# Optimization experiments

Hardware: AMD Instinct MI355X
Metric: run time of the kernel (lower is better)

Reference implementation:

```python
import jax, jax.numpy as jnp
import numpy as np

FIX_SCALE = np.array([[0.,0.,0.],[1.,0.,0.],[0.,1.,0.],[0.,0.,1.],[-1.,0.,0.],[0.,-1.,0.]], dtype=np.float32)
NUM_HEADS = 8
ATTN_DIMS = 512
HEAD_DIMS = ATTN_DIMS // NUM_HEADS
NUM_LEARN = 6
SIG_CLAMP = 9.21  # safe_sigmoid clamp


def quat_to_rotmat(q):
    # q: [G,4] (w,x,y,z), normalized -> [G,3,3]
    q = q / jnp.linalg.norm(q, axis=-1, keepdims=True)
    w, x, y, z = q[..., 0], q[..., 1], q[..., 2], q[..., 3]
    r0 = jnp.stack([1 - 2*(y*y + z*z), 2*(x*y - w*z), 2*(x*z + w*y)], -1)
    r1 = jnp.stack([2*(x*y + w*z), 1 - 2*(x*x + z*z), 2*(y*z - w*x)], -1)
    r2 = jnp.stack([2*(x*z - w*y), 2*(y*z + w*x), 1 - 2*(x*x + y*y)], -1)
    return jnp.stack([r0, r1, r2], -2)


def bilinear_sample(fm, gx, gy):
    # fm: [C,H,W]; gx,gy: [...] in [-1,1]; align_corners=False, zero padding
    C, H, W = fm.shape
    x = (gx + 1.0) * (W * 0.5) - 0.5
    y = (gy + 1.0) * (H * 0.5) - 0.5
    x0 = jnp.floor(x); y0 = jnp.floor(y)
    wx1 = x - x0; wx0 = 1.0 - wx1
    wy1 = y - y0; wy0 = 1.0 - wy1

    def gather(xf, yf):
        xi = xf.astype(jnp.int32); yi = yf.astype(jnp.int32)
        valid = (xi >= 0) & (xi < W) & (yi >= 0) & (yi < H)
        xi = jnp.clip(xi, 0, W - 1); yi = jnp.clip(yi, 0, H - 1)
        return fm[:, yi, xi] * valid[None].astype(fm.dtype)  # [C, ...]

    out = (gather(x0, y0) * (wx0 * wy0)[None]
           + gather(x0 + 1, y0) * (wx1 * wy0)[None]
           + gather(x0, y0 + 1) * (wx0 * wy1)[None]
           + gather(x0 + 1, y0 + 1) * (wx1 * wy1)[None])
    return jnp.moveaxis(out, 0, -1)  # [..., C]


def setup_inputs() -> dict:
    key = jax.random.key(0)
    ks = jax.random.split(key, 16)
    G, BS, GFD = 8192, 1, 32
    means = jax.random.uniform(ks[0], (G, 3), minval=-1.0, maxval=1.0)
    means = means.at[:, 2].add(3.0)  # push in front of camera
    scales = jax.random.uniform(ks[1], (G, 3), minval=0.01, maxval=0.1)
    rotations = jax.random.normal(ks[2], (G, 4))
    features = jax.random.normal(ks[3], (BS, G, 3, GFD))
    transforms = jnp.tile(jnp.eye(4)[None], (G, 1, 1)) + 0.01 * jax.random.normal(ks[4], (G, 4, 4))
    f = 64.0
    proj = jnp.array([[f, 0., 32., 0.], [0., f, 32., 0.], [0., 0., 1., 0.], [0., 0., 0., 1.]], dtype=jnp.float32)
    projection = jnp.tile(proj[None], (BS, 1, 1))
    image_features = jax.random.normal(ks[5], (BS, 256, 64, 64))
    s = lambda d: 1.0 / np.sqrt(d)
    Wq = jax.random.normal(ks[6], (GFD, ATTN_DIMS)) * s(GFD)
    Wk = jax.random.normal(ks[7], (ATTN_DIMS, 256)) * s(256)
    Wv = jax.random.normal(ks[8], (ATTN_DIMS, 256)) * s(256)
    W_off = jax.random.normal(ks[9], (HEAD_DIMS + 3, NUM_LEARN * 3)) * s(HEAD_DIMS + 3)
    b_off = jnp.zeros((NUM_LEARN * 3,))
    Wout = jax.random.normal(ks[10], (ATTN_DIMS, GFD)) * s(ATTN_DIMS)
    b_out = jnp.zeros((GFD,))
    return {"means": means, "scales": scales, "rotations": rotations, "features": features,
            "transforms": transforms, "projection": projection, "image_features": image_features,
            "Wq": Wq, "Wk": Wk, "Wv": Wv, "W_off": W_off, "b_off": b_off, "Wout": Wout, "b_out": b_out}


def reference(means, scales, rotations, features, transforms, projection, image_features,
              Wq, Wk, Wv, W_off, b_off, Wout, b_out):
    G = means.shape[0]
    bs = features.shape[0]
    H, HD = NUM_HEADS, HEAD_DIMS
    h_img, w_img = image_features.shape[-2:]

    # queries: [bs,G,3,attn] -> [bs,H,G,3,hd]
    q_full = jnp.einsum('bgtf,fa->bgta', features, Wq)
    q = q_full.reshape(bs, G, 3, H, HD).transpose(0, 3, 1, 2, 4)

    # transform means to world space with per-gaussian 4x4
    homo = jnp.concatenate([means, jnp.ones((G, 1), means.dtype)], -1)  # [G,4]
    means_w = jnp.einsum('gij,gj->gi', transforms, homo)[:, :3]  # [G,3]

    # OffsetNet: per-head learnable offsets from (world mean, token-mean query)
    q_mean = q.mean(axis=3)  # [bs,H,G,hd]
    m_b = jnp.broadcast_to(means_w[None, None], (bs, H, G, 3))
    off_in = jnp.concatenate([m_b, q_mean], -1)  # [bs,H,G,hd+3]
    learnable = jax.nn.sigmoid(jnp.clip(off_in @ W_off + b_off, -SIG_CLAMP, SIG_CLAMP))
    learnable = learnable.reshape(bs, H, G, NUM_LEARN, 3) - 0.5
    fix = jnp.broadcast_to(jnp.asarray(FIX_SCALE)[None, None, None], (bs, H, G, FIX_SCALE.shape[0], 3))
    scale_all = jnp.concatenate([fix, learnable], axis=-2)  # [bs,H,G,K,3]
    K = scale_all.shape[-2]

    offset_pts = scale_all * scales[None, None, :, None, :]
    RT = jnp.swapaxes(quat_to_rotmat(rotations), -1, -2)  # [G,3,3]
    offset_pts = jnp.einsum('gij,bhgkj->bhgki', RT, offset_pts) + means_w[None, None, :, None, :]

    # project to 2D, normalize to [0,1), then to grid coords [-1,1]
    pts4 = jnp.concatenate([offset_pts, jnp.ones_like(offset_pts[..., :1])], -1)
    p = jnp.einsum('bij,bhgkj->bhgki', projection, pts4)
    p2 = p[..., :2] / jnp.clip(p[..., 2:3], 1e-5)
    wh = jnp.array([w_img, h_img], dtype=p2.dtype)
    pnorm = jnp.clip(p2 / wh, 0.0, 0.9999)
    grid = 2.0 * pnorm - 1.0  # [bs,H,G,K,2]

    # key/value maps via 1x1 conv, split into per-head channel groups
    kmap = jnp.einsum('ac,bchw->bahw', Wk, image_features).reshape(bs, H, HD, h_img, w_img)
    vmap_ = jnp.einsum('ac,bchw->bahw', Wv, image_features).reshape(bs, H, HD, h_img, w_img)

    sample_bh = jax.vmap(jax.vmap(bilinear_sample, in_axes=(0, 0, 0)), in_axes=(0, 0, 0))
    k_s = sample_bh(kmap, grid[..., 0], grid[..., 1])   # [bs,H,G,K,hd]
    v_s = sample_bh(vmap_, grid[..., 0], grid[..., 1])  # [bs,H,G,K,hd]

    scale = HD ** -0.5
    scores = jnp.einsum('bhgid,bhgkd->bhgik', q, k_s) * scale
    attn = jax.nn.softmax(scores, axis=-1)
    out = jnp.einsum('bhgik,bhgkd->bhgid', attn, v_s)  # [bs,H,G,3,hd]
    out = out.transpose(0, 2, 3, 1, 4).reshape(bs, G, 3, H * HD)  # b g i (h d)
    out = out @ Wout + b_out
    return out + features
```

## Files before the change

### kernel.cpp

```cpp
#include <hip/hip_runtime.h>
#include <hip/hip_bf16.h>
#include <hip/hip_fp16.h>

typedef _Float16 half2v __attribute__((ext_vector_type(2)));
typedef _Float16 half8v __attribute__((ext_vector_type(8)));
typedef __attribute__((ext_vector_type(4))) float float4v;

__device__ __forceinline__ half2v u2h(unsigned u) { return __builtin_bit_cast(half2v, u); }
__device__ __forceinline__ unsigned h2u(half2v h) { return __builtin_bit_cast(unsigned, h); }
__device__ __forceinline__ unsigned short f2hu(float f) {
    _Float16 h = (_Float16)f; return __builtin_bit_cast(unsigned short, h);
}
__device__ __forceinline__ unsigned packh(float lo, float hi) {
    half2v h; h[0] = (_Float16)lo; h[1] = (_Float16)hi; return h2u(h);
}
__device__ __forceinline__ void ld8h(const unsigned short* p, float* f) {
    uint4 u = *(const uint4*)p;
    half2v h0 = u2h(u.x), h1 = u2h(u.y), h2 = u2h(u.z), h3 = u2h(u.w);
    f[0] = (float)h0[0]; f[1] = (float)h0[1]; f[2] = (float)h1[0]; f[3] = (float)h1[1];
    f[4] = (float)h2[0]; f[5] = (float)h2[1]; f[6] = (float)h3[0]; f[7] = (float)h3[1];
}

__global__ __launch_bounds__(256) void offmlp_kernel(
    const float* __restrict__ means, const float* __restrict__ transforms,
    const float* __restrict__ features, const float* __restrict__ Wq,
    const float* __restrict__ W_off, const float* __restrict__ b_off,
    float* __restrict__ lrn_all)
{
    __shared__ __attribute__((aligned(16))) unsigned short Wq16[32 * 512];
    __shared__ float Woffs[1224];
    __shared__ float Wc[36][144];
    __shared__ float A[32][38];
    const int tid = threadIdx.x;
    const int g0 = blockIdx.x * 32;

#pragma unroll
    for (int i = 0; i < 16; i++) {
        int idx4 = i * 256 + tid;
        float4 v = ((const float4*)Wq)[idx4];
        unsigned* dst = (unsigned*)&Wq16[idx4 * 4];
        dst[0] = packh(v.x, v.y);
        dst[1] = packh(v.z, v.w);
    }
    for (int i = tid; i < 1206; i += 256) Woffs[i] = W_off[i];
    if (tid < 18) Woffs[1206 + tid] = b_off[tid];
    {
        const int gi = tid >> 3, sl = tid & 7;
        const int g = g0 + gi;
        const float* fb = features + (size_t)g * 96 + sl * 4;
        float4 t0 = *(const float4*)(fb);
        float4 t1 = *(const float4*)(fb + 32);
        float4 t2 = *(const float4*)(fb + 64);
        A[gi][3 + sl * 4 + 0] = (t0.x + t1.x + t2.x) * (1.f / 3.f);
        A[gi][3 + sl * 4 + 1] = (t0.y + t1.y + t2.y) * (1.f / 3.f);
        A[gi][3 + sl * 4 + 2] = (t0.z + t1.z + t2.z) * (1.f / 3.f);
        A[gi][3 + sl * 4 + 3] = (t0.w + t1.w + t2.w) * (1.f / 3.f);
        if (sl < 3) {
            const float* T = transforms + (size_t)g * 16 + sl * 4;
            float m0 = means[(size_t)g * 3];
            float m1 = means[(size_t)g * 3 + 1];
            float m2 = means[(size_t)g * 3 + 2];
            A[gi][sl] = T[0] * m0 + T[1] * m1 + T[2] * m2 + T[3];
        } else if (sl == 3) {
            A[gi][35] = 1.f;
        }
    }
    __syncthreads();

    for (int k = 0; k < 21; k++) {
        int oi = k * 256 + tid;
        if (oi < 5184) {
            int j = oi / 144, c = oi - j * 144;
            int h = c / 18, l = c - h * 18;
            float v;
            if (j < 3) {
                v = Woffs[j * 18 + l];
            } else if (j == 35) {
                v = Woffs[1206 + l];
            } else {
                int f = j - 3;
                const unsigned* wq2 = (const unsigned*)&Wq16[f * 512 + h * 64];
                float s = 0.f;
#pragma unroll
                for (int d2 = 0; d2 < 32; d2++) {
                    half2v w2 = u2h(wq2[d2]);
                    s += (float)w2[0] * Woffs[(3 + 2 * d2) * 18 + l]
                       + (float)w2[1] * Woffs[(4 + 2 * d2) * 18 + l];
                }
                v = s;
            }
            Wc[j][c] = v;
        }
    }
    __syncthreads();

#pragma unroll
    for (int k = 0; k < 18; k++) {
        int oi = k * 256 + tid;
        int gi = oi / 144, c = oi - gi * 144;
        float s = 0.f;
#pragma unroll
        for (int j = 0; j < 36; j++) s += A[gi][j] * Wc[j][c];
        s = fminf(fmaxf(s, -9.21f), 9.21f);
        lrn_all[(size_t)(g0 + gi) * 144 + c] = 1.f / (1.f + expf(-s)) - 0.5f;
    }
}

__global__ __launch_bounds__(256) void conv_fused_kernel(
    const float* __restrict__ img, const float* __restrict__ Wk,
    const float* __restrict__ Wv, unsigned short* __restrict__ buf)
{
    __shared__ __attribute__((aligned(16))) unsigned short Bt[64][264];
    __shared__ __attribute__((aligned(16))) unsigned short Wt[64][264];
    const int tid = threadIdx.x;
    const int p0 = blockIdx.x * 64;

#pragma unroll
    for (int i = 0; i < 4; i++) {
        int chunk = i * 256 + tid;
        int kp  = chunk >> 3;
        int pxg = (chunk & 7) * 8;
        const float* r0 = img + (size_t)(2 * kp) * 4096 + p0 + pxg;
        const float* r1 = img + (size_t)(2 * kp + 1) * 4096 + p0 + pxg;
        float4 a0 = *(const float4*)r0, a1 = *(const float4*)(r0 + 4);
        float4 b0 = *(const float4*)r1, b1 = *(const float4*)(r1 + 4);
        unsigned lo[8], hi[8];
        lo[0] = f2hu(a0.x); lo[1] = f2hu(a0.y); lo[2] = f2hu(a0.z); lo[3] = f2hu(a0.w);
        lo[4] = f2hu(a1.x); lo[5] = f2hu(a1.y); lo[6] = f2hu(a1.z); lo[7] = f2hu(a1.w);
        hi[0] = f2hu(b0.x); hi[1] = f2hu(b0.y); hi[2] = f2hu(b0.z); hi[3] = f2hu(b0.w);
        hi[4] = f2hu(b1.x); hi[5] = f2hu(b1.y); hi[6] = f2hu(b1.z); hi[7] = f2hu(b1.w);
#pragma unroll
        for (int j = 0; j < 8; j++)
            *(unsigned*)&Bt[pxg + j][2 * kp] = lo[j] | (hi[j] << 16);
    }

    const int w = tid >> 6, l = tid & 63;
    const int m = l & 15, quad = l >> 4;
    const int mrow = w * 16 + m;

#pragma unroll
    for (int j = 0; j < 2; j++) {
        const int o0 = blockIdx.y * 128 + j * 64;
        const float* Wsel = (o0 < 512) ? Wk : Wv;
        const int obase = (o0 < 512) ? o0 : (o0 - 512);
        if (j) __syncthreads();
        {
            const int row = tid >> 2, q = tid & 3;
            const float* wp = Wsel + (size_t)(obase + row) * 256 + q * 64;
#pragma unroll
            for (int jj = 0; jj < 8; jj++) {
                float4 w0 = *(const float4*)(wp + jj * 8);
                float4 w1 = *(const float4*)(wp + jj * 8 + 4);
                uint4 pk;
                pk.x = packh(w0.x, w0.y); pk.y = packh(w0.z, w0.w);
                pk.z = packh(w1.x, w1.y); pk.w = packh(w1.z, w1.w);
                *(uint4*)&Wt[row][q * 64 + jj * 8] = pk;
            }
        }
        __syncthreads();

        float4v acc[4] = {{0,0,0,0},{0,0,0,0},{0,0,0,0},{0,0,0,0}};
#pragma unroll
        for (int kk = 0; kk < 8; kk++) {
            const int kofs = kk * 32 + quad * 8;
            half8v af = *(const half8v*)&Bt[mrow][kofs];
#pragma unroll
            for (int nt = 0; nt < 4; nt++) {
                half8v b8 = *(const half8v*)&Wt[nt * 16 + m][kofs];
                acc[nt] = __builtin_amdgcn_mfma_f32_16x16x32_f16(af, b8, acc[nt], 0, 0, 0);
            }
        }
#pragma unroll
        for (int nt = 0; nt < 4; nt++) {
#pragma unroll
            for (int r = 0; r < 4; r++) {
                size_t px = p0 + w * 16 + quad * 4 + r;
                buf[px * 1024 + o0 + nt * 16 + m] = f2hu(acc[nt][r]);
            }
        }
    }
}

__global__ __launch_bounds__(256) void qgemm_kernel(
    const float* __restrict__ features, const float* __restrict__ Wq,
    unsigned short* __restrict__ qfull)
{
    __shared__ __attribute__((aligned(16))) unsigned short WqT[256][40];
    const int tid = threadIdx.x;
    const int R0 = blockIdx.x * 64;
    const int n0 = blockIdx.y * 256;
#pragma unroll
    for (int k = 0; k < 32; k++)
        WqT[tid][k] = f2hu(Wq[(size_t)k * 512 + n0 + tid]);
    __syncthreads();

    const int w = tid >> 6, l = tid & 63, m = l & 15, quad = l >> 4;
    const int row = R0 + w * 16 + m;
    const float* fp = features + (size_t)row * 32 + quad * 8;
    float4 f0 = *(const float4*)fp, f1 = *(const float4*)(fp + 4);
    half8v af;
    af[0] = (_Float16)f0.x; af[1] = (_Float16)f0.y;
    af[2] = (_Float16)f0.z; af[3] = (_Float16)f0.w;
    af[4] = (_Float16)f1.x; af[5] = (_Float16)f1.y;
    af[6] = (_Float16)f1.z; af[7] = (_Float16)f1.w;
    float4v acc[16];
#pragma unroll
    for (int t = 0; t < 16; t++) acc[t] = (float4v){0.f, 0.f, 0.f, 0.f};
#pragma unroll
    for (int t = 0; t < 16; t++) {
        half8v b8 = *(const half8v*)&WqT[t * 16 + m][quad * 8];
        acc[t] = __builtin_amdgcn_mfma_f32_16x16x32_f16(af, b8, acc[t], 0, 0, 0);
    }
    const int rb = R0 + w * 16 + quad * 4;
#pragma unroll
    for (int t = 0; t < 16; t++)
#pragma unroll
        for (int r = 0; r < 4; r++)
            qfull[(size_t)(rb + r) * 512 + n0 + t * 16 + m] = f2hu(acc[t][r]);
}

__global__ __launch_bounds__(256, 4) void attn_core_kernel(
    const float* __restrict__ means, const float* __restrict__ scales,
    const float* __restrict__ rot,   const float* __restrict__ transforms,
    const float* __restrict__ projection, const float* __restrict__ lrn_all,
    const unsigned short* __restrict__ buf, unsigned short* __restrict__ qfull)
{
    __shared__ __attribute__((aligned(16))) unsigned qf2[768];
    __shared__ __attribute__((aligned(16))) unsigned vsh2[3072];
    __shared__ __attribute__((aligned(16))) uint4 pixwt[96];
    __shared__ __attribute__((aligned(16))) unsigned att2[288];
    __shared__ __attribute__((aligned(16))) float lrnsh[144];
    __shared__ float mw[3], sc3[3], Rt[9], pr[12];

    const int g = blockIdx.x, tid = threadIdx.x;

    if (tid < 36) {
        ((float4*)lrnsh)[tid] = ((const float4*)(lrn_all + (size_t)g * 144))[tid];
    }
    if (tid >= 64 && tid < 67) {
        sc3[tid - 64] = scales[(size_t)g * 3 + (tid - 64)];
    } else if (tid >= 68 && tid < 80) {
        pr[tid - 68] = projection[tid - 68];
    } else if (tid == 80) {
        float w = rot[(size_t)g * 4],     x = rot[(size_t)g * 4 + 1];
        float y = rot[(size_t)g * 4 + 2], z = rot[(size_t)g * 4 + 3];
        float n = rsqrtf(w * w + x * x + y * y + z * z);
        w *= n; x *= n; y *= n; z *= n;
        float R00 = 1 - 2 * (y * y + z * z), R01 = 2 * (x * y - w * z), R02 = 2 * (x * z + w * y);
        float R10 = 2 * (x * y + w * z), R11 = 1 - 2 * (x * x + z * z), R12 = 2 * (y * z - w * x);
        float R20 = 2 * (x * z - w * y), R21 = 2 * (y * z + w * x), R22 = 1 - 2 * (x * x + y * y);
        Rt[0] = R00; Rt[1] = R10; Rt[2] = R20;
        Rt[3] = R01; Rt[4] = R11; Rt[5] = R21;
        Rt[6] = R02; Rt[7] = R12; Rt[8] = R22;
    } else if (tid >= 84 && tid < 87) {
        int i = tid - 84;
        float m0 = means[(size_t)g * 3];
        float m1 = means[(size_t)g * 3 + 1];
        float m2 = means[(size_t)g * 3 + 2];
        const float* T = transforms + (size_t)g * 16 + i * 4;
        mw[i] = T[0] * m0 + T[1] * m1 + T[2] * m2 + T[3];
    }
    {
        const unsigned* qsrc = (const unsigned*)(qfull + (size_t)g * 1536);
#pragma unroll
        for (int i = 0; i < 3; i++) qf2[tid + i * 256] = qsrc[tid + i * 256];
    }
    __syncthreads();

    if (tid < 96) {
        int h = tid / 12, k = tid % 12;
        float s0, s1, s2;
        if (k < 6) {
            const float FSx[6] = {0.f, 1.f, 0.f, 0.f, -1.f, 0.f};
            const float FSy[6] = {0.f, 0.f, 1.f, 0.f, 0.f, -1.f};
            const float FSz[6] = {0.f, 0.f, 0.f, 1.f, 0.f, 0.f};
            s0 = FSx[k]; s1 = FSy[k]; s2 = FSz[k];
        } else {
            int b = h * 18 + (k - 6) * 3;
            s0 = lrnsh[b]; s1 = lrnsh[b + 1]; s2 = lrnsh[b + 2];
        }
        float o0 = s0 * sc3[0], o1 = s1 * sc3[1], o2 = s2 * sc3[2];
        float wx = Rt[0] * o0 + Rt[1] * o1 + Rt[2] * o2 + mw[0];
        float wy = Rt[3] * o0 + Rt[4] * o1 + Rt[5] * o2 + mw[1];
        float wz = Rt[6] * o0 + Rt[7] * o1 + Rt[8] * o2 + mw[2];
        float px = pr[0] * wx + pr[1] * wy + pr[2]  * wz + pr[3];
        float py = pr[4] * wx + pr[5] * wy + pr[6]  * wz + pr[7];
        float pz = pr[8] * wx + pr[9] * wy + pr[10] * wz + pr[11];
        pz = fmaxf(pz, 1e-5f);
        float gx = fminf(fmaxf(px / pz * (1.f / 64.f), 0.f), 0.9999f);
        float gy = fminf(fmaxf(py / pz * (1.f / 64.f), 0.f), 0.9999f);
        float x = gx * 64.f - 0.5f, y = gy * 64.f - 0.5f;
        float fx = floorf(x), fy = floorf(y);
        int x0 = (int)fx, y0 = (int)fy;
        float wx1 = x - fx, wy1 = y - fy;
        float wx0 = 1.f - wx1, wy0 = 1.f - wy1;
        int xs[2] = {x0, x0 + 1}, ys[2] = {y0, y0 + 1};
        float wxs[2] = {wx0, wx1}, wys[2] = {wy0, wy1};
        unsigned pix[4]; float wf[4];
#pragma unroll
        for (int c = 0; c < 4; c++) {
            int xi = xs[c & 1], yi = ys[c >> 1];
            bool v = ((unsigned)xi < 64u) & ((unsigned)yi < 64u);
            int xc = min(max(xi, 0), 63), yc = min(max(yi, 0), 63);
            pix[c] = (unsigned)(yc * 64 + xc);
            wf[c] = v ? wxs[c & 1] * wys[c >> 1] : 0.f;
        }
        uint4 pw;
        pw.x = pix[0] | (pix[1] << 16);
        pw.y = pix[2] | (pix[3] << 16);
        pw.z = packh(wf[0], wf[1]);
        pw.w = packh(wf[2], wf[3]);
        pixwt[tid] = pw;
// ... 72 lines not shown
    if (tid < 24) {
        float*    row  = (float*)att2 + tid * 12;
        unsigned* rowp = att2 + tid * 12;
        float m = row[0];
#pragma unroll
        for (int k = 1; k < 12; k++) m = fmaxf(m, row[k]);
        float e_[12]; float ssum = 0.f;
#pragma unroll
        for (int k = 0; k < 12; k++) { e_[k] = expf(row[k] - m); ssum += e_[k]; }
        float inv = 1.f / ssum;
#pragma unroll
        for (int k = 0; k < 12; k++) { float a = e_[k] * inv; rowp[k] = packh(a, a); }
    }
    __syncthreads();

    {
        unsigned* oa32 = (unsigned*)(qfull + (size_t)g * 1536);
#pragma unroll
        for (int i = 0; i < 3; i++) {
            int e = tid + i * 256;
            int t = e >> 8, a2p = e & 255;
            int h = a2p >> 5, ddp = a2p & 31;
            const unsigned* ar2 = att2 + (h * 3 + t) * 12;
            const unsigned* vp  = vsh2 + h * 12 * 32 + ddp;
            half2v acc = {0, 0};
#pragma unroll
            for (int k = 0; k < 12; k++)
                acc += u2h(ar2[k]) * u2h(vp[k * 32]);
            oa32[e] = h2u(acc);
        }
    }
}

__global__ __launch_bounds__(256, 6) void attn_core_basic(
    const float* __restrict__ means, const float* __restrict__ scales,
    const float* __restrict__ rot,   const float* __restrict__ transforms,
    const float* __restrict__ projection, const float* __restrict__ W_off,
    const float* __restrict__ b_off, const unsigned short* __restrict__ buf,
    unsigned short* __restrict__ qfull)
{
    __shared__ __attribute__((aligned(16))) unsigned qf2[768];
    __shared__ __attribute__((aligned(16))) unsigned vsh2[3072];
    __shared__ __attribute__((aligned(16))) float qm_u[512];
    __shared__ __attribute__((aligned(16))) unsigned att2[288];
    __shared__ float mw[3], sc3[3], Rt[9], pr[12];

    float* lrn  = (float*)att2;
    float* wofl = (float*)vsh2;
    float* bofl = wofl + 1206;

    const int g = blockIdx.x, tid = threadIdx.x;

    for (int i = tid; i < 1206; i += 256) wofl[i] = W_off[i];
    if (tid < 18) bofl[tid] = b_off[tid];
    if (tid >= 32 && tid < 35) {
        sc3[tid - 32] = scales[(size_t)g * 3 + (tid - 32)];
    } else if (tid >= 36 && tid < 48) {
        pr[tid - 36] = projection[tid - 36];
    } else if (tid == 48) {
        float w = rot[(size_t)g * 4],     x = rot[(size_t)g * 4 + 1];
        float y = rot[(size_t)g * 4 + 2], z = rot[(size_t)g * 4 + 3];
        float n = rsqrtf(w * w + x * x + y * y + z * z);
        w *= n; x *= n; y *= n; z *= n;
        float R00 = 1 - 2 * (y * y + z * z), R01 = 2 * (x * y - w * z), R02 = 2 * (x * z + w * y);
        float R10 = 2 * (x * y + w * z), R11 = 1 - 2 * (x * x + z * z), R12 = 2 * (y * z - w * x);
        float R20 = 2 * (x * z - w * y), R21 = 2 * (y * z + w * x), R22 = 1 - 2 * (x * x + y * y);
// ... 12 lines not shown
        const unsigned* qsrc = (const unsigned*)(qfull + (size_t)g * 1536);
#pragma unroll
        for (int i = 0; i < 3; i++) qf2[tid + i * 256] = qsrc[tid + i * 256];
    }
    __syncthreads();

    {
        half2v a = u2h(qf2[tid]), b = u2h(qf2[256 + tid]), c = u2h(qf2[512 + tid]);
        qm_u[tid * 2]     = ((float)a[0] + (float)b[0] + (float)c[0]) * (1.f / 3.f);
        qm_u[tid * 2 + 1] = ((float)a[1] + (float)b[1] + (float)c[1]) * (1.f / 3.f);
    }
    __syncthreads();

    if (tid < 144) {
        int h = tid / 18, l = tid % 18;
        float s = bofl[l];
#pragma unroll
        for (int i = 0; i < 3; i++) s += mw[i] * wofl[i * 18 + l];
        for (int d = 0; d < 64; d++) s += qm_u[h * 64 + d] * wofl[(3 + d) * 18 + l];
        s = fminf(fmaxf(s, -9.21f), 9.21f);
        lrn[tid] = 1.f / (1.f + expf(-s)) - 0.5f;
    }
    __syncthreads();

    if (tid < 96) {
        int h = tid / 12, k = tid % 12;
        float s0, s1, s2;
        if (k < 6) {
            const float FSx[6] = {0.f, 1.f, 0.f, 0.f, -1.f, 0.f};
            const float FSy[6] = {0.f, 0.f, 1.f, 0.f, 0.f, -1.f};
            const float FSz[6] = {0.f, 0.f, 0.f, 1.f, 0.f, 0.f};
            s0 = FSx[k]; s1 = FSy[k]; s2 = FSz[k];
        } else {
            int b = h * 18 + (k - 6) * 3;
            s0 = lrn[b]; s1 = lrn[b + 1]; s2 = lrn[b + 2];
        }
        float o0 = s0 * sc3[0], o1 = s1 * sc3[1], o2 = s2 * sc3[2];
        float wx = Rt[0] * o0 + Rt[1] * o1 + Rt[2] * o2 + mw[0];
        float wy = Rt[3] * o0 + Rt[4] * o1 + Rt[5] * o2 + mw[1];
        float wz = Rt[6] * o0 + Rt[7] * o1 + Rt[8] * o2 + mw[2];
        float px = pr[0] * wx + pr[1] * wy + pr[2]  * wz + pr[3];
        float py = pr[4] * wx + pr[5] * wy + pr[6]  * wz + pr[7];
        float pz = pr[8] * wx + pr[9] * wy + pr[10] * wz + pr[11];
        pz = fmaxf(pz, 1e-5f);
        float gx = fminf(fmaxf(px / pz * (1.f / 64.f), 0.f), 0.9999f);
        float gy = fminf(fmaxf(py / pz * (1.f / 64.f), 0.f), 0.9999f);
        float x = gx * 64.f - 0.5f, y = gy * 64.f - 0.5f;
        float fx = floorf(x), fy = floorf(y);
        int x0 = (int)fx, y0 = (int)fy;
        float wx1 = x - fx, wy1 = y - fy;
        float wx0 = 1.f - wx1, wy0 = 1.f - wy1;
        int xs[2] = {x0, x0 + 1}, ys[2] = {y0, y0 + 1};
        float wxs[2] = {wx0, wx1}, wys[2] = {wy0, wy1};
        unsigned pix[4]; float wf[4];
#pragma unroll
        for (int c = 0; c < 4; c++) {
            int xi = xs[c & 1], yi = ys[c >> 1];
            bool v = ((unsigned)xi < 64u) & ((unsigned)yi < 64u);
            int xc = min(max(xi, 0), 63), yc = min(max(yi, 0), 63);
            pix[c] = (unsigned)(yc * 64 + xc);
            wf[c] = v ? wxs[c & 1] * wys[c >> 1] : 0.f;
        }
        uint4 pw;
        pw.x = pix[0] | (pix[1] << 16);
        pw.y = pix[2] | (pix[3] << 16);
        pw.z = packh(wf[0], wf[1]);
        pw.w = packh(wf[2], wf[3]);
        ((uint4*)qm_u)[tid] = pw;
// ... 72 lines not shown
    if (tid < 24) {
        float*    row  = (float*)att2 + tid * 12;
        unsigned* rowp = att2 + tid * 12;
        float m = row[0];
#pragma unroll
        for (int k = 1; k < 12; k++) m = fmaxf(m, row[k]);
        float e_[12]; float ssum = 0.f;
#pragma unroll
        for (int k = 0; k < 12; k++) { e_[k] = expf(row[k] - m); ssum += e_[k]; }
        float inv = 1.f / ssum;
#pragma unroll
        for (int k = 0; k < 12; k++) { float a = e_[k] * inv; rowp[k] = packh(a, a); }
    }
    __syncthreads();

    {
        unsigned* oa32 = (unsigned*)(qfull + (size_t)g * 1536);
#pragma unroll
        for (int i = 0; i < 3; i++) {
            int e = tid + i * 256;
            int t = e >> 8, a2p = e & 255;
            int h = a2p >> 5, ddp = a2p & 31;
            const unsigned* ar2 = att2 + (h * 3 + t) * 12;
            const unsigned* vp  = vsh2 + h * 12 * 32 + ddp;
            half2v acc = {0, 0};
#pragma unroll
            for (int k = 0; k < 12; k++)
                acc += u2h(ar2[k]) * u2h(vp[k * 32]);
            oa32[e] = h2u(acc);
        }
    }
}

__global__ __launch_bounds__(256) void outgemm_kernel(
    const unsigned short* __restrict__ oa, const float* __restrict__ Wout,
    const float* __restrict__ b_out, const float* __restrict__ features,
    float* __restrict__ out)
{
    __shared__ __attribute__((aligned(16))) unsigned short WT[32][520];
    const int tid = threadIdx.x;
    const int R0 = blockIdx.x * 64;
#pragma unroll
    for (int j = 0; j < 64; j++) {
        int lin = j * 256 + tid;
        WT[lin & 31][lin >> 5] = f2hu(Wout[lin]);
    }
    __syncthreads();

    const int w = tid >> 6, l = tid & 63, m = l & 15, quad = l >> 4;
    const int row = R0 + w * 16 + m;
    float4v acc[2] = {{0,0,0,0},{0,0,0,0}};
#pragma unroll
    for (int kk = 0; kk < 16; kk++) {
        half8v af = *(const half8v*)(oa + (size_t)row * 512 + kk * 32 + quad * 8);
#pragma unroll
        for (int t = 0; t < 2; t++) {
            half8v b8 = *(const half8v*)&WT[t * 16 + m][kk * 32 + quad * 8];
            acc[t] = __builtin_amdgcn_mfma_f32_16x16x32_f16(af, b8, acc[t], 0, 0, 0);
        }
    }
    const int rb = R0 + w * 16 + quad * 4;
#pragma unroll
    for (int t = 0; t < 2; t++) {
        int col = t * 16 + m;
        float bb = b_out[col];
#pragma unroll
        for (int r = 0; r < 4; r++) {
            int rr = rb + r;
            out[(size_t)rr * 32 + col] = acc[t][r] + bb + features[(size_t)rr * 32 + col];
        }
    }
}

__global__ __launch_bounds__(256, 6) void attn_fused_kernel(
    const float* __restrict__ means, const float* __restrict__ scales,
    const float* __restrict__ rot,   const float* __restrict__ features,
    const float* __restrict__ transforms, const float* __restrict__ projection,
    const float* __restrict__ Wq,    const float* __restrict__ W_off,
    const float* __restrict__ b_off, const float* __restrict__ Wout,
    const float* __restrict__ b_out, const unsigned short* __restrict__ buf,
    float* __restrict__ out)
{
    __shared__ float feat[96];
    __shared__ __attribute__((aligned(16))) float qf[1536];
    __shared__ float qm[512];
    __shared__ float mw[3], sc3[3], Rt[9], pr[12];
    __shared__ float lrn[144];
    __shared__ int   coff[96][4];
    __shared__ float cwt[96][4];
    __shared__ __attribute__((aligned(16))) char pool[12288];
    __shared__ float att[288];

    unsigned short* vsh = (unsigned short*)pool;
    const int g = blockIdx.x, tid = threadIdx.x;

    if (tid < 96) {
        feat[tid] = features[(size_t)g * 96 + tid];
    } else if (tid < 99) {
        sc3[tid - 96] = scales[(size_t)g * 3 + (tid - 96)];
    } else if (tid >= 100 && tid < 112) {
        pr[tid - 100] = projection[tid - 100];
    } else if (tid == 112) {
        float w = rot[(size_t)g * 4],     x = rot[(size_t)g * 4 + 1];
        float y = rot[(size_t)g * 4 + 2], z = rot[(size_t)g * 4 + 3];
        float n = rsqrtf(w * w + x * x + y * y + z * z);
        w *= n; x *= n; y *= n; z *= n;
// ... 24 lines not shown
            s10 += f1 * w2.x; s11 += f1 * w2.y;
            s20 += f2 * w2.x; s21 += f2 * w2.y;
        }
        *(float2*)(qf + a0)        = make_float2(s00, s01);
        *(float2*)(qf + 512 + a0)  = make_float2(s10, s11);
        *(float2*)(qf + 1024 + a0) = make_float2(s20, s21);
    }
    __syncthreads();

    qm[tid]       = (qf[tid]       + qf[tid + 512] + qf[tid + 1024]) * (1.f / 3.f);
    qm[tid + 256] = (qf[tid + 256] + qf[tid + 768] + qf[tid + 1280]) * (1.f / 3.f);
    __syncthreads();

    if (tid < 144) {
        int h = tid / 18, l = tid % 18;
        float s = b_off[l];
#pragma unroll
        for (int i = 0; i < 3; i++) s += mw[i] * W_off[i * 18 + l];
        for (int d = 0; d < 64; d++) s += qm[h * 64 + d] * W_off[(size_t)(3 + d) * 18 + l];
        s = fminf(fmaxf(s, -9.21f), 9.21f);
        lrn[tid] = 1.f / (1.f + expf(-s)) - 0.5f;
    }
    __syncthreads();

    if (tid < 96) {
        int h = tid / 12, k = tid % 12;
        float s0, s1, s2;
        if (k < 6) {
            const float FSx[6] = {0.f, 1.f, 0.f, 0.f, -1.f, 0.f};
            const float FSy[6] = {0.f, 0.f, 1.f, 0.f, 0.f, -1.f};
            const float FSz[6] = {0.f, 0.f, 0.f, 1.f, 0.f, 0.f};
            s0 = FSx[k]; s1 = FSy[k]; s2 = FSz[k];
        } else {
            int b = h * 18 + (k - 6) * 3;
            s0 = lrn[b]; s1 = lrn[b + 1]; s2 = lrn[b + 2];
        }
        float o0 = s0 * sc3[0], o1 = s1 * sc3[1], o2 = s2 * sc3[2];
        float wx = Rt[0] * o0 + Rt[1] * o1 + Rt[2] * o2 + mw[0];
        float wy = Rt[3] * o0 + Rt[4] * o1 + Rt[5] * o2 + mw[1];
        float wz = Rt[6] * o0 + Rt[7] * o1 + Rt[8] * o2 + mw[2];
        float px = pr[0] * wx + pr[1] * wy + pr[2]  * wz + pr[3];
        float py = pr[4] * wx + pr[5] * wy + pr[6]  * wz + pr[7];
        float pz = pr[8] * wx + pr[9] * wy + pr[10] * wz + pr[11];
        pz = fmaxf(pz, 1e-5f);
        float gx = fminf(fmaxf(px / pz * (1.f / 64.f), 0.f), 0.9999f);
        float gy = fminf(fmaxf(py / pz * (1.f / 64.f), 0.f), 0.9999f);
        float x = gx * 64.f - 0.5f, y = gy * 64.f - 0.5f;
        float fx = floorf(x), fy = floorf(y);
        int x0 = (int)fx, y0 = (int)fy;
        float wx1 = x - fx, wx0c = 1.f - wx1;
        float wy1 = y - fy, wy0c = 1.f - wy1;
        int xs[2] = {x0, x0 + 1}, ys[2] = {y0, y0 + 1};
        float wxs[2] = {wx0c, wx1}, wys[2] = {wy0c, wy1};
#pragma unroll
        for (int c = 0; c < 4; c++) {
            int dx = c & 1, dy = c >> 1;
            int xi = xs[dx], yi = ys[dy];
            bool v = (xi >= 0) & (xi < 64) & (yi >= 0) & (yi < 64);
            int xc = min(max(xi, 0), 63), yc = min(max(yi, 0), 63);
            coff[tid][c] = (yc * 64 + xc) * 1024;
            cwt[tid][c]  = v ? wxs[dx] * wys[dy] : 0.f;
        }
    }
    __syncthreads();

    {
        const int slice = tid & 7, d0 = slice * 8, grp = tid >> 3;
#pragma unroll
// ... 96 lines not shown
            for (int s = 0; s < 16; s++) acc += red[(s * 3 + t) * 32 + c];
            out[(size_t)g * 96 + tid] = acc;
        }
    }
}

extern "C" void kernel_launch(void* const* d_in, const int* in_sizes, int n_in,
                              void* d_out, int out_size, void* d_ws, size_t ws_size,
                              hipStream_t stream) {
    const float* means      = (const float*)d_in[0];
    const float* scales     = (const float*)d_in[1];
    const float* rot        = (const float*)d_in[2];
    const float* features   = (const float*)d_in[3];
    const float* transforms = (const float*)d_in[4];
    const float* projection = (const float*)d_in[5];
    const float* img        = (const float*)d_in[6];
    const float* Wq         = (const float*)d_in[7];
    const float* Wk         = (const float*)d_in[8];
    const float* Wv         = (const float*)d_in[9];
    const float* W_off      = (const float*)d_in[10];
    const float* b_off      = (const float*)d_in[11];
    const float* Wout       = (const float*)d_in[12];
    const float* b_out      = (const float*)d_in[13];
    float* out = (float*)d_out;

    char* w = (char*)d_ws;
    unsigned short* buf = (unsigned short*)(w + 64);
    const size_t BUF_BYTES = (size_t)4096 * 1024 * 2;
    const size_t Q_BYTES   = (size_t)24576 * 512 * 2;
    const size_t LRN_BYTES = (size_t)8192 * 144 * 4;
    const size_t need  = 64 + BUF_BYTES + Q_BYTES;
    const size_t need2 = need + LRN_BYTES;

    dim3 gridc(64, 8);
    conv_fused_kernel<<<gridc, 256, 0, stream>>>(img, Wk, Wv, buf);

    if (ws_size >= need2) {
        unsigned short* qfull = (unsigned short*)(w + 64 + BUF_BYTES);
        float* lrn_all = (float*)(w + 64 + BUF_BYTES + Q_BYTES);

        offmlp_kernel<<<256, 256, 0, stream>>>(
            means, transforms, features, Wq, W_off, b_off, lrn_all);
        dim3 gridq(384, 2);
        qgemm_kernel<<<gridq, 256, 0, stream>>>(features, Wq, qfull);
        attn_core_kernel<<<8192, 256, 0, stream>>>(
            means, scales, rot, transforms, projection, lrn_all, buf, qfull);
        outgemm_kernel<<<384, 256, 0, stream>>>(qfull, Wout, b_out, features, out);
    } else if (ws_size >= need) {
        unsigned short* qfull = (unsigned short*)(w + 64 + BUF_BYTES);
        dim3 gridq(384, 2);
        qgemm_kernel<<<gridq, 256, 0, stream>>>(features, Wq, qfull);
        attn_core_basic<<<8192, 256, 0, stream>>>(
            means, scales, rot, transforms, projection, W_off, b_off, buf, qfull);
        outgemm_kernel<<<384, 256, 0, stream>>>(qfull, Wout, b_out, features, out);
    } else {
        attn_fused_kernel<<<8192, 256, 0, stream>>>(
            means, scales, rot, features, transforms, projection,
            Wq, W_off, b_off, Wout, b_out, buf, out);
    }
}
```

Before: 182.0 us.

## Merge offset-MLP and Q GEMM into one launch; split conv over more blocks

Merges the offset-MLP and Q-projection GEMM into one kernel, with block ranges dispatching to either path through a shared memory pool. The offset part now uses 64 blocks that each handle 128 gaussians, so the folded Wq·W_off weight matrix is built fewer times. The conv kernel now does one 64-output tile per block on a 64x16 grid instead of two tiles per block, giving more blocks and no inner barrier. The trade-offs are one fewer launch but a larger shared-memory footprint for every block of the merged kernel, and the image tile is now reloaded by twice as many blocks.

```diff
diff --git a/kernel.cpp b/kernel.cpp
--- a/kernel.cpp
+++ b/kernel.cpp
@@ -19,91 +19,6 @@
     half2v h0 = u2h(u.x), h1 = u2h(u.y), h2 = u2h(u.z), h3 = u2h(u.w);
     f[0] = (float)h0[0]; f[1] = (float)h0[1]; f[2] = (float)h1[0]; f[3] = (float)h1[1];
     f[4] = (float)h2[0]; f[5] = (float)h2[1]; f[6] = (float)h3[0]; f[7] = (float)h3[1];
-}
-
-__global__ __launch_bounds__(256) void offmlp_kernel(
-    const float* __restrict__ means, const float* __restrict__ transforms,
-    const float* __restrict__ features, const float* __restrict__ Wq,
-    const float* __restrict__ W_off, const float* __restrict__ b_off,
-    float* __restrict__ lrn_all)
-{
-    __shared__ __attribute__((aligned(16))) unsigned short Wq16[32 * 512];
-    __shared__ float Woffs[1224];
-    __shared__ float Wc[36][144];
-    __shared__ float A[32][38];
-    const int tid = threadIdx.x;
-    const int g0 = blockIdx.x * 32;
-
-#pragma unroll
-    for (int i = 0; i < 16; i++) {
-        int idx4 = i * 256 + tid;
-        float4 v = ((const float4*)Wq)[idx4];
-        unsigned* dst = (unsigned*)&Wq16[idx4 * 4];
-        dst[0] = packh(v.x, v.y);
-        dst[1] = packh(v.z, v.w);
-    }
-    for (int i = tid; i < 1206; i += 256) Woffs[i] = W_off[i];
-    if (tid < 18) Woffs[1206 + tid] = b_off[tid];
-    {
-        const int gi = tid >> 3, sl = tid & 7;
-        const int g = g0 + gi;
-        const float* fb = features + (size_t)g * 96 + sl * 4;
-        float4 t0 = *(const float4*)(fb);
-        float4 t1 = *(const float4*)(fb + 32);
-        float4 t2 = *(const float4*)(fb + 64);
-        A[gi][3 + sl * 4 + 0] = (t0.x + t1.x + t2.x) * (1.f / 3.f);
-        A[gi][3 + sl * 4 + 1] = (t0.y + t1.y + t2.y) * (1.f / 3.f);
-        A[gi][3 + sl * 4 + 2] = (t0.z + t1.z + t2.z) * (1.f / 3.f);
-        A[gi][3 + sl * 4 + 3] = (t0.w + t1.w + t2.w) * (1.f / 3.f);
-        if (sl < 3) {
-            const float* T = transforms + (size_t)g * 16 + sl * 4;
-            float m0 = means[(size_t)g * 3];
-            float m1 = means[(size_t)g * 3 + 1];
-            float m2 = means[(size_t)g * 3 + 2];
-            A[gi][sl] = T[0] * m0 + T[1] * m1 + T[2] * m2 + T[3];
-        } else if (sl == 3) {
-            A[gi][35] = 1.f;
-        }
-    }
-    __syncthreads();
-
-    for (int k = 0; k < 21; k++) {
-        int oi = k * 256 + tid;
-        if (oi < 5184) {
-            int j = oi / 144, c = oi - j * 144;
-            int h = c / 18, l = c - h * 18;
-            float v;
-            if (j < 3) {
-                v = Woffs[j * 18 + l];
-            } else if (j == 35) {
-                v = Woffs[1206 + l];
-            } else {
-                int f = j - 3;
-                const unsigned* wq2 = (const unsigned*)&Wq16[f * 512 + h * 64];
-                float s = 0.f;
-#pragma unroll
-                for (int d2 = 0; d2 < 32; d2++) {
-                    half2v w2 = u2h(wq2[d2]);
-                    s += (float)w2[0] * Woffs[(3 + 2 * d2) * 18 + l]
-                       + (float)w2[1] * Woffs[(4 + 2 * d2) * 18 + l];
-                }
-                v = s;
-            }
-            Wc[j][c] = v;
-        }
-    }
-    __syncthreads();
-
-#pragma unroll
-    for (int k = 0; k < 18; k++) {
-        int oi = k * 256 + tid;
-        int gi = oi / 144, c = oi - gi * 144;
-        float s = 0.f;
-#pragma unroll
-        for (int j = 0; j < 36; j++) s += A[gi][j] * Wc[j][c];
-        s = fminf(fmaxf(s, -9.21f), 9.21f);
-        lrn_all[(size_t)(g0 + gi) * 144 + c] = 1.f / (1.f + expf(-s)) - 0.5f;
-    }
 }
 
 __global__ __launch_bounds__(256) void conv_fused_kernel(
@@ -114,6 +29,9 @@
     __shared__ __attribute__((aligned(16))) unsigned short Wt[64][264];
     const int tid = threadIdx.x;
     const int p0 = blockIdx.x * 64;
+    const int o0 = blockIdx.y * 64;
+    const float* Wsel = (o0 < 512) ? Wk : Wv;
+    const int obase = (o0 < 512) ? o0 : (o0 - 512);
 
 #pragma unroll
     for (int i = 0; i < 4; i++) {
@@ -133,90 +51,169 @@
         for (int j = 0; j < 8; j++)
             *(unsigned*)&Bt[pxg + j][2 * kp] = lo[j] | (hi[j] << 16);
     }
+    {
+        const int row = tid >> 2, q = tid & 3;
+        const float* wp = Wsel + (size_t)(obase + row) * 256 + q * 64;
+#pragma unroll
+        for (int j = 0; j < 8; j++) {
+            float4 w0 = *(const float4*)(wp + j * 8);
+            float4 w1 = *(const float4*)(wp + j * 8 + 4);
+            uint4 pk;
+            pk.x = packh(w0.x, w0.y); pk.y = packh(w0.z, w0.w);
+            pk.z = packh(w1.x, w1.y); pk.w = packh(w1.z, w1.w);
+            *(uint4*)&Wt[row][q * 64 + j * 8] = pk;
+        }
+    }
+    __syncthreads();
 
     const int w = tid >> 6, l = tid & 63;
     const int m = l & 15, quad = l >> 4;
     const int mrow = w * 16 + m;
 
-#pragma unroll
-    for (int j = 0; j < 2; j++) {
-        const int o0 = blockIdx.y * 128 + j * 64;
-        const float* Wsel = (o0 < 512) ? Wk : Wv;
-        const int obase = (o0 < 512) ? o0 : (o0 - 512);
-        if (j) __syncthreads();
-        {
-            const int row = tid >> 2, q = tid & 3;
-            const float* wp = Wsel + (size_t)(obase + row) * 256 + q * 64;
-#pragma unroll
-            for (int jj = 0; jj < 8; jj++) {
-                float4 w0 = *(const float4*)(wp + jj * 8);
-                float4 w1 = *(const float4*)(wp + jj * 8 + 4);
-                uint4 pk;
-                pk.x = packh(w0.x, w0.y); pk.y = packh(w0.z, w0.w);
-                pk.z = packh(w1.x, w1.y); pk.w = packh(w1.z, w1.w);
-                *(uint4*)&Wt[row][q * 64 + jj * 8] = pk;
-            }
-        }
+    float4v acc[4] = {{0,0,0,0},{0,0,0,0},{0,0,0,0},{0,0,0,0}};
+#pragma unroll
+    for (int kk = 0; kk < 8; kk++) {
+        const int kofs = kk * 32 + quad * 8;
+        half8v af = *(const half8v*)&Bt[mrow][kofs];
+#pragma unroll
+        for (int nt = 0; nt < 4; nt++) {
+            half8v b8 = *(const half8v*)&Wt[nt * 16 + m][kofs];
+            acc[nt] = __builtin_amdgcn_mfma_f32_16x16x32_f16(af, b8, acc[nt], 0, 0, 0);
+        }
+    }
+#pragma unroll
+    for (int nt = 0; nt < 4; nt++) {
+#pragma unroll
+        for (int r = 0; r < 4; r++) {
+            size_t px = p0 + w * 16 + quad * 4 + r;
+            buf[px * 1024 + o0 + nt * 16 + m] = f2hu(acc[nt][r]);
+        }
+    }
+}
+
+__global__ __launch_bounds__(256) void qoff_kernel(
+    const float* __restrict__ features, const float* __restrict__ Wq,
+    const float* __restrict__ means, const float* __restrict__ transforms,
+    const float* __restrict__ W_off, const float* __restrict__ b_off,
+    unsigned short* __restrict__ qfull, float* __restrict__ lrn_all)
+{
+    __shared__ __attribute__((aligned(16))) char POOL[63264];
+    const int tid = threadIdx.x;
+    const int b = blockIdx.x;
+
+    if (b < 768) {
+        unsigned short (*WqT)[40] = (unsigned short (*)[40])POOL;
+        const int R0 = (b >> 1) * 64;
+        const int n0 = (b & 1) * 256;
+#pragma unroll
+        for (int k = 0; k < 32; k++)
+            WqT[tid][k] = f2hu(Wq[(size_t)k * 512 + n0 + tid]);
         __syncthreads();
 
-        float4v acc[4] = {{0,0,0,0},{0,0,0,0},{0,0,0,0},{0,0,0,0}};
-#pragma unroll
-        for (int kk = 0; kk < 8; kk++) {
-            const int kofs = kk * 32 + quad * 8;
-            half8v af = *(const half8v*)&Bt[mrow][kofs];
-#pragma unroll
-            for (int nt = 0; nt < 4; nt++) {
-                half8v b8 = *(const half8v*)&Wt[nt * 16 + m][kofs];
-                acc[nt] = __builtin_amdgcn_mfma_f32_16x16x32_f16(af, b8, acc[nt], 0, 0, 0);
-            }
-        }
-#pragma unroll
-        for (int nt = 0; nt < 4; nt++) {
-#pragma unroll
-            for (int r = 0; r < 4; r++) {
-                size_t px = p0 + w * 16 + quad * 4 + r;
-                buf[px * 1024 + o0 + nt * 16 + m] = f2hu(acc[nt][r]);
-            }
-        }
-    }
-}
-
-__global__ __launch_bounds__(256) void qgemm_kernel(
-    const float* __restrict__ features, const float* __restrict__ Wq,
-    unsigned short* __restrict__ qfull)
-{
-    __shared__ __attribute__((aligned(16))) unsigned short WqT[256][40];
-    const int tid = threadIdx.x;
-    const int R0 = blockIdx.x * 64;
-    const int n0 = blockIdx.y * 256;
-#pragma unroll
-    for (int k = 0; k < 32; k++)
-        WqT[tid][k] = f2hu(Wq[(size_t)k * 512 + n0 + tid]);
-    __syncthreads();
-
-    const int w = tid >> 6, l = tid & 63, m = l & 15, quad = l >> 4;
-    const int row = R0 + w * 16 + m;
-    const float* fp = features + (size_t)row * 32 + quad * 8;
-    float4 f0 = *(const float4*)fp, f1 = *(const float4*)(fp + 4);
-    half8v af;
-    af[0] = (_Float16)f0.x; af[1] = (_Float16)f0.y;
-    af[2] = (_Float16)f0.z; af[3] = (_Float16)f0.w;
-    af[4] = (_Float16)f1.x; af[5] = (_Float16)f1.y;
-    af[6] = (_Float16)f1.z; af[7] = (_Float16)f1.w;
-    float4v acc[16];
-#pragma unroll
-    for (int t = 0; t < 16; t++) acc[t] = (float4v){0.f, 0.f, 0.f, 0.f};
-#pragma unroll
-    for (int t = 0; t < 16; t++) {
-        half8v b8 = *(const half8v*)&WqT[t * 16 + m][quad * 8];
-        acc[t] = __builtin_amdgcn_mfma_f32_16x16x32_f16(af, b8, acc[t], 0, 0, 0);
-    }
-    const int rb = R0 + w * 16 + quad * 4;
-#pragma unroll
-    for (int t = 0; t < 16; t++)
-#pragma unroll
-        for (int r = 0; r < 4; r++)
-            qfull[(size_t)(rb + r) * 512 + n0 + t * 16 + m] = f2hu(acc[t][r]);
+        const int w = tid >> 6, l = tid & 63, m = l & 15, quad = l >> 4;
+        const int row = R0 + w * 16 + m;
+        const float* fp = features + (size_t)row * 32 + quad * 8;
+        float4 f0 = *(const float4*)fp, f1 = *(const float4*)(fp + 4);
+        half8v af;
+        af[0] = (_Float16)f0.x; af[1] = (_Float16)f0.y;
+        af[2] = (_Float16)f0.z; af[3] = (_Float16)f0.w;
+        af[4] = (_Float16)f1.x; af[5] = (_Float16)f1.y;
+        af[6] = (_Float16)f1.z; af[7] = (_Float16)f1.w;
+        float4v acc[16];
+#pragma unroll
+        for (int t = 0; t < 16; t++) acc[t] = (float4v){0.f, 0.f, 0.f, 0.f};
+#pragma unroll
+        for (int t = 0; t < 16; t++) {
+            half8v b8 = *(const half8v*)&WqT[t * 16 + m][quad * 8];
+            acc[t] = __builtin_amdgcn_mfma_f32_16x16x32_f16(af, b8, acc[t], 0, 0, 0);
+        }
+        const int rb = R0 + w * 16 + quad * 4;
+#pragma unroll
+        for (int t = 0; t < 16; t++)
+#pragma unroll
+            for (int r = 0; r < 4; r++)
+                qfull[(size_t)(rb + r) * 512 + n0 + t * 16 + m] = f2hu(acc[t][r]);
+    } else {
+        unsigned short* Wq16 = (unsigned short*)POOL;
+        float* Woffs = (float*)(POOL + 32768);
+        float (*Wc)[144] = (float (*)[144])(POOL + 37664);
+        float (*A)[38]   = (float (*)[38])(POOL + 58400);
+        const int blk = b - 768;
+
+        for (int i = 0; i < 16; i++) {
+            int idx4 = i * 256 + tid;
+            float4 v = ((const float4*)Wq)[idx4];
+            unsigned* dst = (unsigned*)&Wq16[idx4 * 4];
+            dst[0] = packh(v.x, v.y);
+            dst[1] = packh(v.z, v.w);
+        }
+        for (int i = tid; i < 1206; i += 256) Woffs[i] = W_off[i];
+        if (tid < 18) Woffs[1206 + tid] = b_off[tid];
+        __syncthreads();
+
+        for (int k = 0; k < 21; k++) {
+            int oi = k * 256 + tid;
+            if (oi < 5184) {
+                int j = oi / 144, c = oi - j * 144;
+                int h = c / 18, l = c - h * 18;
+                float v;
+                if (j < 3) {
+                    v = Woffs[j * 18 + l];
+                } else if (j == 35) {
+                    v = Woffs[1206 + l];
+                } else {
+                    int f = j - 3;
+                    const unsigned* wq2 = (const unsigned*)&Wq16[f * 512 + h * 64];
+                    float s = 0.f;
+#pragma unroll
+                    for (int d2 = 0; d2 < 32; d2++) {
+                        half2v w2 = u2h(wq2[d2]);
+                        s += (float)w2[0] * Woffs[(3 + 2 * d2) * 18 + l]
+                           + (float)w2[1] * Woffs[(4 + 2 * d2) * 18 + l];
+                    }
+                    v = s;
+                }
+                Wc[j][c] = v;
+            }
+        }
+        __syncthreads();
+
+        for (int ch = 0; ch < 4; ch++) {
+            const int g0 = blk * 128 + ch * 32;
+            {
+                const int gi = tid >> 3, sl = tid & 7;
+                const int g = g0 + gi;
+                const float* fb = features + (size_t)g * 96 + sl * 4;
+                float4 t0 = *(const float4*)(fb);
+                float4 t1 = *(const float4*)(fb + 32);
+                float4 t2 = *(const float4*)(fb + 64);
+                A[gi][3 + sl * 4 + 0] = (t0.x + t1.x + t2.x) * (1.f / 3.f);
+                A[gi][3 + sl * 4 + 1] = (t0.y + t1.y + t2.y) * (1.f / 3.f);
+                A[gi][3 + sl * 4 + 2] = (t0.z + t1.z + t2.z) * (1.f / 3.f);
+                A[gi][3 + sl * 4 + 3] = (t0.w + t1.w + t2.w) * (1.f / 3.f);
+                if (sl < 3) {
+                    const float* T = transforms + (size_t)g * 16 + sl * 4;
+                    float m0 = means[(size_t)g * 3];
+                    float m1 = means[(size_t)g * 3 + 1];
+                    float m2 = means[(size_t)g * 3 + 2];
+                    A[gi][sl] = T[0] * m0 + T[1] * m1 + T[2] * m2 + T[3];
+                } else if (sl == 3) {
+                    A[gi][35] = 1.f;
+                }
+            }
+            __syncthreads();
+            for (int k = 0; k < 18; k++) {
+                int oi = k * 256 + tid;
+                int gi = oi / 144, c = oi - gi * 144;
+                float s = 0.f;
+#pragma unroll
+                for (int j = 0; j < 36; j++) s += A[gi][j] * Wc[j][c];
+                s = fminf(fmaxf(s, -9.21f), 9.21f);
+                lrn_all[(size_t)(g0 + gi) * 144 + c] = 1.f / (1.f + expf(-s)) - 0.5f;
+            }
+            __syncthreads();
+        }
+    }
 }
 
 __global__ __launch_bounds__(256, 4) void attn_core_kernel(
@@ -276,8 +273,8 @@
             const float FSz[6] = {0.f, 0.f, 0.f, 1.f, 0.f, 0.f};
             s0 = FSx[k]; s1 = FSy[k]; s2 = FSz[k];
         } else {
-            int b = h * 18 + (k - 6) * 3;
-            s0 = lrnsh[b]; s1 = lrnsh[b + 1]; s2 = lrnsh[b + 2];
+            int bq = h * 18 + (k - 6) * 3;
+            s0 = lrnsh[bq]; s1 = lrnsh[bq + 1]; s2 = lrnsh[bq + 2];
         }
         float o0 = s0 * sc3[0], o1 = s1 * sc3[1], o2 = s2 * sc3[2];
         float wx = Rt[0] * o0 + Rt[1] * o1 + Rt[2] * o2 + mw[0];
@@ -416,6 +413,84 @@
     }
 }
 
+__global__ __launch_bounds__(256) void outgemm_kernel(
+    const unsigned short* __restrict__ oa, const float* __restrict__ Wout,
+    const float* __restrict__ b_out, const float* __restrict__ features,
+    float* __restrict__ out)
+{
+    __shared__ __attribute__((aligned(16))) unsigned short WT[32][520];
+    const int tid = threadIdx.x;
+    const int R0 = blockIdx.x * 64;
+#pragma unroll
+    for (int j = 0; j < 64; j++) {
+        int lin = j * 256 + tid;
+        WT[lin & 31][lin >> 5] = f2hu(Wout[lin]);
+    }
+    __syncthreads();
+
+    const int w = tid >> 6, l = tid & 63, m = l & 15, quad = l >> 4;
+    const int row = R0 + w * 16 + m;
+    float4v acc[2] = {{0,0,0,0},{0,0,0,0}};
+#pragma unroll
+    for (int kk = 0; kk < 16; kk++) {
+        half8v af = *(const half8v*)(oa + (size_t)row * 512 + kk * 32 + quad * 8);
+#pragma unroll
+        for (int t = 0; t < 2; t++) {
+            half8v b8 = *(const half8v*)&WT[t * 16 + m][kk * 32 + quad * 8];
+            acc[t] = __builtin_amdgcn_mfma_f32_16x16x32_f16(af, b8, acc[t], 0, 0, 0);
+        }
+    }
+    const int rb = R0 + w * 16 + quad * 4;
+#pragma unroll
+    for (int t = 0; t < 2; t++) {
+        int col = t * 16 + m;
+        float bb = b_out[col];
+#pragma unroll
+        for (int r = 0; r < 4; r++) {
+            int rr = rb + r;
+            out[(size_t)rr * 32 + col] = acc[t][r] + bb + features[(size_t)rr * 32 + col];
+        }
+    }
+}
+
+__global__ __launch_bounds__(256) void qgemm_kernel(
+    const float* __restrict__ features, const float* __restrict__ Wq,
+    unsigned short* __restrict__ qfull)
+{
+    __shared__ __attribute__((aligned(16))) unsigned short WqT[256][40];
+    const int tid = threadIdx.x;
+    const int R0 = blockIdx.x * 64;
+    const int n0 = blockIdx.y * 256;
+#pragma unroll
+    for (int k = 0; k < 32; k++)
+        WqT[tid][k] = f2hu(Wq[(size_t)k * 512 + n0 + tid]);
+    __syncthreads();
+
+    const int w = tid >> 6, l = tid & 63, m = l & 15, quad = l >> 4;
+    const int row = R0 + w * 16 + m;
+    const float* fp = features + (size_t)row * 32 + quad * 8;
+    float4 f0 = *(const float4*)fp, f1 = *(const float4*)(fp + 4);
+    half8v af;
+    af[0] = (_Float16)f0.x; af[1] = (_Float16)f0.y;
+    af[2] = (_Float16)f0.z; af[3] = (_Float16)f0.w;
+    af[4] = (_Float16)f1.x; af[5] = (_Float16)f1.y;
+    af[6] = (_Float16)f1.z; af[7] = (_Float16)f1.w;
+    float4v acc[16];
+#pragma unroll
+    for (int t = 0; t < 16; t++) acc[t] = (float4v){0.f, 0.f, 0.f, 0.f};
+#pragma unroll
+    for (int t = 0; t < 16; t++) {
+        half8v b8 = *(const half8v*)&WqT[t * 16 + m][quad * 8];
+        acc[t] = __builtin_amdgcn_mfma_f32_16x16x32_f16(af, b8, acc[t], 0, 0, 0);
+    }
+    const int rb = R0 + w * 16 + quad * 4;
+#pragma unroll
+    for (int t = 0; t < 16; t++)
+#pragma unroll
+        for (int r = 0; r < 4; r++)
+            qfull[(size_t)(rb + r) * 512 + n0 + t * 16 + m] = f2hu(acc[t][r]);
+}
+
 __global__ __launch_bounds__(256, 6) void attn_core_basic(
     const float* __restrict__ means, const float* __restrict__ scales,
     const float* __restrict__ rot,   const float* __restrict__ transforms,
@@ -494,8 +569,8 @@
             const float FSz[6] = {0.f, 0.f, 0.f, 1.f, 0.f, 0.f};
             s0 = FSx[k]; s1 = FSy[k]; s2 = FSz[k];
         } else {
-            int b = h * 18 + (k - 6) * 3;
-            s0 = lrn[b]; s1 = lrn[b + 1]; s2 = lrn[b + 2];
+            int bq = h * 18 + (k - 6) * 3;
+            s0 = lrn[bq]; s1 = lrn[bq + 1]; s2 = lrn[bq + 2];
         }
         float o0 = s0 * sc3[0], o1 = s1 * sc3[1], o2 = s2 * sc3[2];
         float wx = Rt[0] * o0 + Rt[1] * o1 + Rt[2] * o2 + mw[0];
@@ -634,46 +709,6 @@
     }
 }
 
-__global__ __launch_bounds__(256) void outgemm_kernel(
-    const unsigned short* __restrict__ oa, const float* __restrict__ Wout,
-    const float* __restrict__ b_out, const float* __restrict__ features,
-    float* __restrict__ out)
-{
-    __shared__ __attribute__((aligned(16))) unsigned short WT[32][520];
-    const int tid = threadIdx.x;
-    const int R0 = blockIdx.x * 64;
-#pragma unroll
-    for (int j = 0; j < 64; j++) {
-        int lin = j * 256 + tid;
-        WT[lin & 31][lin >> 5] = f2hu(Wout[lin]);
-    }
-    __syncthreads();
-
-    const int w = tid >> 6, l = tid & 63, m = l & 15, quad = l >> 4;
-    const int row = R0 + w * 16 + m;
-    float4v acc[2] = {{0,0,0,0},{0,0,0,0}};
-#pragma unroll
-    for (int kk = 0; kk < 16; kk++) {
-        half8v af = *(const half8v*)(oa + (size_t)row * 512 + kk * 32 + quad * 8);
-#pragma unroll
-        for (int t = 0; t < 2; t++) {
-            half8v b8 = *(const half8v*)&WT[t * 16 + m][kk * 32 + quad * 8];
-            acc[t] = __builtin_amdgcn_mfma_f32_16x16x32_f16(af, b8, acc[t], 0, 0, 0);
-        }
-    }
-    const int rb = R0 + w * 16 + quad * 4;
-#pragma unroll
-    for (int t = 0; t < 2; t++) {
-        int col = t * 16 + m;
-        float bb = b_out[col];
-#pragma unroll
-        for (int r = 0; r < 4; r++) {
-            int rr = rb + r;
-            out[(size_t)rr * 32 + col] = acc[t][r] + bb + features[(size_t)rr * 32 + col];
-        }
-    }
-}
-
 __global__ __launch_bounds__(256, 6) void attn_fused_kernel(
     const float* __restrict__ means, const float* __restrict__ scales,
     const float* __restrict__ rot,   const float* __restrict__ features,
@@ -764,8 +799,8 @@
             const float FSz[6] = {0.f, 0.f, 0.f, 1.f, 0.f, 0.f};
             s0 = FSx[k]; s1 = FSy[k]; s2 = FSz[k];
         } else {
-            int b = h * 18 + (k - 6) * 3;
-            s0 = lrn[b]; s1 = lrn[b + 1]; s2 = lrn[b + 2];
+            int bq = h * 18 + (k - 6) * 3;
+            s0 = lrn[bq]; s1 = lrn[bq + 1]; s2 = lrn[bq + 2];
         }
         float o0 = s0 * sc3[0], o1 = s1 * sc3[1], o2 = s2 * sc3[2];
         float wx = Rt[0] * o0 + Rt[1] * o1 + Rt[2] * o2 + mw[0];
@@ -928,17 +963,15 @@
     const size_t need  = 64 + BUF_BYTES + Q_BYTES;
     const size_t need2 = need + LRN_BYTES;
 
-    dim3 gridc(64, 8);
+    dim3 gridc(64, 16);
     conv_fused_kernel<<<gridc, 256, 0, stream>>>(img, Wk, Wv, buf);
 
     if (ws_size >= need2) {
         unsigned short* qfull = (unsigned short*)(w + 64 + BUF_BYTES);
         float* lrn_all = (float*)(w + 64 + BUF_BYTES + Q_BYTES);
 
-        offmlp_kernel<<<256, 256, 0, stream>>>(
-            means, transforms, features, Wq, W_off, b_off, lrn_all);
-        dim3 gridq(384, 2);
-        qgemm_kernel<<<gridq, 256, 0, stream>>>(features, Wq, qfull);
+        qoff_kernel<<<832, 256, 0, stream>>>(
+            features, Wq, means, transforms, W_off, b_off, qfull, lrn_all);
         attn_core_kernel<<<8192, 256, 0, stream>>>(
             means, scales, rot, transforms, projection, lrn_all, buf, qfull);
         outgemm_kernel<<<384, 256, 0, stream>>>(qfull, Wout, b_out, features, out);
```

After: 205.5 us. 1.13x slower.
